# Performance work log

Measured on AMD Instinct MI355X. Metric: run time of the kernel, lower is better.

The kernel has to match this reference:

```python
import jax, jax.numpy as jnp
import numpy as np

NUM_NODES = 20000
NUM_EDGES = 65536
WIDTH = 64
EDGE_FEAT = 6
HIDDEN = 128


def setup_inputs() -> dict:
    key = jax.random.key(0)
    ks = jax.random.split(key, 6)
    x = jax.random.normal(ks[0], (NUM_NODES, WIDTH), dtype=jnp.float32)
    edge_attr = jax.random.normal(ks[1], (NUM_EDGES, EDGE_FEAT), dtype=jnp.float32)
    # weight-generating MLP params (the `nn` callable), fan-in scaled
    W1 = jax.random.normal(ks[2], (EDGE_FEAT, HIDDEN), dtype=jnp.float32) / np.sqrt(EDGE_FEAT)
    b1 = jnp.zeros((HIDDEN,), dtype=jnp.float32)
    W2 = jax.random.normal(ks[3], (HIDDEN, WIDTH * WIDTH), dtype=jnp.float32) / np.sqrt(HIDDEN)
    b2 = jnp.zeros((WIDTH * WIDTH,), dtype=jnp.float32)
    senders = jax.random.randint(ks[4], (NUM_EDGES,), 0, NUM_NODES)
    receivers = jax.random.randint(ks[5], (NUM_EDGES,), 0, NUM_NODES)
    return {"x": x, "edge_attr": edge_attr, "W1": W1, "b1": b1,
            "W2": W2, "b2": b2, "senders": senders, "receivers": receivers}


def reference(x, edge_attr, W1, b1, W2, b2, senders, receivers):
    n_segs, width = x.shape
    # nn(edge_attr): (E, width*width) edge-conditioned weights
    h = jax.nn.relu(edge_attr @ W1 + b1)
    weight = (h @ W2 + b2).reshape(-1, width, width)  # (E, w, w)
    # gather sender features, per-edge (1,w) @ (w,w) matmul -> (E, w)
    msgs = jnp.einsum('ew,ewv->ev', x[senders], weight)
    # scatter-sum messages into receiver nodes (aggr == 'sum')
    return jax.ops.segment_sum(msgs, receivers, num_segments=n_segs)
```

## Files before the change

kernel.cpp:

```cpp
#include <hip/hip_runtime.h>
#include <stdint.h>

typedef _Float16 f16;
typedef f16 f16x8 __attribute__((ext_vector_type(8)));
typedef float f32x4 __attribute__((ext_vector_type(4)));

#define NUM_NODES 20000
#define NUM_EDGES 65536
#define WIDTH 64
#define EDGE_FEAT 6
#define HIDDEN 128
#define BM 256
#define NCHUNK 129
#define XPAD 72

#define XH_HALFS (NUM_NODES * WIDTH)
#define XCONV_BLKS 625
#define W2G_HALFS (NCHUNK * 4096)
#define HT_HALFS ((size_t)NCHUNK * NUM_EDGES)
#define HBLKS (NUM_EDGES / 256)
#define OUT_FLOATS (NUM_NODES * WIDTH)
#define ZBLKS 313

__device__ __forceinline__ void gload_lds16(const f16* g, f16* l) {
  __builtin_amdgcn_global_load_lds(
      (const __attribute__((address_space(1))) unsigned int*)g,
      (__attribute__((address_space(3))) unsigned int*)l, 16, 0, 0);
}

__global__ __launch_bounds__(256) void prep_kernel(
    const float* __restrict__ x, const float* __restrict__ W2,
    const float* __restrict__ b2, const float* __restrict__ ea,
    const float* __restrict__ W1, const float* __restrict__ b1,
    f16* __restrict__ ws_h, float* __restrict__ out, int use_ht)
{
  f16* x_h = ws_h;
  f16* W2g = ws_h + XH_HALFS;
  f16* hT  = ws_h + XH_HALFS + W2G_HALFS;
  const int blk = blockIdx.x, tid = threadIdx.x;

  if (blk < NCHUNK) {
    __shared__ float row[4096];
    const int ki = blk;
    const float* srcrow;
    if (ki < HIDDEN) {
      const float4* src = (const float4*)(W2 + (size_t)ki * 4096);
      #pragma unroll
      for (int i = 0; i < 4; ++i) {
        float4 v = src[tid + 256 * i];
        *(float4*)&row[(tid + 256 * i) * 4] = v;
      }
      __syncthreads();
      srcrow = row;
    } else {
      srcrow = b2;
    }
    const int obase = tid * 16;
    f16x8 outv0, outv1;
    #pragma unroll
    for (int u = 0; u < 8; ++u) {
      int o = obase + u;
      int n = o >> 6, pg = (o >> 3) & 7, j = o & 7;
      int k = (pg ^ (n & 7)) * 8 + j;
      outv0[u] = (f16)srcrow[k * 64 + n];
    }
    #pragma unroll
    for (int u = 0; u < 8; ++u) {
      int o = obase + 8 + u;
      int n = o >> 6, pg = (o >> 3) & 7, j = o & 7;
      int k = (pg ^ (n & 7)) * 8 + j;
      outv1[u] = (f16)srcrow[k * 64 + n];
    }
    *(f16x8*)&W2g[(size_t)ki * 4096 + obase] = outv0;
    *(f16x8*)&W2g[(size_t)ki * 4096 + obase + 8] = outv1;
  } else if (blk < NCHUNK + XCONV_BLKS) {
    int idx = (blk - NCHUNK) * 2048 + tid * 8;
    if (idx + 8 <= XH_HALFS) {
      float4 a = *(const float4*)(x + idx);
      float4 b = *(const float4*)(x + idx + 4);
      f16x8 hv;
      hv[0] = (f16)a.x; hv[1] = (f16)a.y; hv[2] = (f16)a.z; hv[3] = (f16)a.w;
      hv[4] = (f16)b.x; hv[5] = (f16)b.y; hv[6] = (f16)b.z; hv[7] = (f16)b.w;
      *(f16x8*)&x_h[idx] = hv;
    }
  } else if (blk < NCHUNK + XCONV_BLKS + ZBLKS) {
    int base = (blk - NCHUNK - XCONV_BLKS) * 4096 + tid * 16;
    float4 z = {0.f, 0.f, 0.f, 0.f};
    #pragma unroll
    for (int i = 0; i < 4; ++i) {
      int idx = base + i * 4;
      if (idx + 4 <= OUT_FLOATS) *(float4*)(out + idx) = z;
    }
  } else if (use_ht) {
    __shared__ float w1s[EDGE_FEAT * HIDDEN];
    __shared__ float b1s[HIDDEN];
    for (int i = tid; i < EDGE_FEAT * HIDDEN; i += 256) w1s[i] = W1[i];
    if (tid < HIDDEN) b1s[tid] = b1[tid];
    __syncthreads();
    const int e = (blk - NCHUNK - XCONV_BLKS - ZBLKS) * 256 + tid;
    const float* p = ea + (size_t)e * EDGE_FEAT;
    float a[6];
    #pragma unroll
    for (int f = 0; f < 6; ++f) a[f] = p[f];
    #pragma unroll 4
    for (int k = 0; k < HIDDEN; ++k) {
      float s = b1s[k];
      #pragma unroll
      for (int f = 0; f < 6; ++f) s = fmaf(a[f], w1s[f * HIDDEN + k], s);
      hT[(size_t)k * NUM_EDGES + e] = (f16)fmaxf(s, 0.f);
    }
    hT[(size_t)HIDDEN * NUM_EDGES + e] = (f16)1.f;
  }
}

template<int HT>
__global__ __launch_bounds__(256, 1) void nnconv_kernel(
    const float* __restrict__ ea, const float* __restrict__ W1,
    const float* __restrict__ b1, const int* __restrict__ senders,
    const int* __restrict__ receivers, const f16* __restrict__ ws_h,
    float* __restrict__ out)
{
  const f16* x_h = ws_h;
  const f16* W2g = ws_h + XH_HALFS;
  const f16* hT  = ws_h + XH_HALFS + W2G_HALFS;
  __shared__ __align__(16) f16 xt[BM][XPAD];
  __shared__ __align__(16) f16 Bb[2][4096];

  const int tid = threadIdx.x;
  const int lane = tid & 63, wid = tid >> 6;
  const int quad = lane >> 4, l15 = lane & 15;
  const int e0 = blockIdx.x * BM;
  const int rowbase = wid * 64;

  {
    int s = senders[e0 + tid];
    const uint4* src = (const uint4*)(x_h + (size_t)s * WIDTH);
    uint4* dst = (uint4*)&xt[tid][0];
    #pragma unroll
    for (int i = 0; i < 8; ++i) dst[i] = src[i];
  }

  float ear[4][6];
  if (!HT) {
    #pragma unroll
    for (int t = 0; t < 4; ++t) {
      const float* p = ea + (size_t)(e0 + rowbase + t * 16 + l15) * EDGE_FEAT;
      #pragma unroll
      for (int f = 0; f < 6; ++f) ear[t][f] = p[f];
    }
  }

  int boff[2][4];
  #pragma unroll
  for (int kc = 0; kc < 2; ++kc)
    #pragma unroll
    for (int nt = 0; nt < 4; ++nt) {
      int n = nt * 16 + l15;
      int g = kc * 4 + quad;
      boff[kc][nt] = n * 64 + (g ^ (n & 7)) * 8;
    }

  const int hrow = e0 + rowbase + l15;
  const int stg_src = wid * 512 + (lane << 3);
  const int stg_dst = wid * 512;

  gload_lds16(W2g + stg_src, &Bb[0][stg_dst]);
  gload_lds16(W2g + 2048 + stg_src, &Bb[0][stg_dst + 2048]);
  gload_lds16(W2g + 4096 + stg_src, &Bb[1][stg_dst]);
  gload_lds16(W2g + 4096 + 2048 + stg_src, &Bb[1][stg_dst + 2048]);
  f16 hA[4], hB[4], hC[4];
  if (HT) {
    const f16* h0 = hT + hrow;
    const f16* h1 = hT + (size_t)NUM_EDGES + hrow;
    #pragma unroll
    for (int t = 0; t < 4; ++t) { hA[t] = h0[t * 16]; hB[t] = h1[t * 16]; }
  }

  __syncthreads();

  f16x8 xf[4][2];
  #pragma unroll
  for (int t = 0; t < 4; ++t)
    #pragma unroll
    for (int kc = 0; kc < 2; ++kc)
      xf[t][kc] = *(const f16x8*)&xt[rowbase + t * 16 + l15][kc * 32 + quad * 8];

  f32x4 acc[4][4];
  #pragma unroll
  for (int t = 0; t < 4; ++t)
    #pragma unroll
    for (int nt = 0; nt < 4; ++nt)
      acc[t][nt] = (f32x4){0.f, 0.f, 0.f, 0.f};

  f16x8 bfA[2][4], bfB[2][4];
  #pragma unroll
  for (int kc = 0; kc < 2; ++kc)
    #pragma unroll
    for (int nt = 0; nt < 4; ++nt)
      bfA[kc][nt] = *(const f16x8*)&Bb[0][boff[kc][nt]];

#define NN_STEP(K, CUR, NXT, DOREAD)                                          \
  {                                                                           \
    asm volatile("s_waitcnt vmcnt(%0) lgkmcnt(0)\n\ts_barrier"                \
                 :: "i"(HT ? 4 : 0) : "memory");                              \
    const int c2_ = ((K) + 2 <= 128) ? (K) + 2 : 128;                         \
    {                                                                         \
      const f16* src_ = W2g + (size_t)c2_ * 4096 + stg_src;                   \
      f16* dst_ = &Bb[(K) & 1][stg_dst];                                      \
      gload_lds16(src_, dst_);                                                \
      gload_lds16(src_ + 2048, dst_ + 2048);                                  \
    }                                                                         \
    __builtin_amdgcn_sched_barrier(0);      \
    if (HT) {                                                                 \
      const f16* hp_ = hT + (size_t)c2_ * NUM_EDGES + hrow;                   \
      hC[0] = hp_[0]; hC[1] = hp_[16]; hC[2] = hp_[32]; hC[3] = hp_[48];      \
    }                                                                         \
    if (DOREAD) {                                                             \
      f16* rb_ = &Bb[((K) + 1) & 1][0];                                       \
      _Pragma("unroll") for (int kc = 0; kc < 2; ++kc)                        \
        _Pragma("unroll") for (int nt = 0; nt < 4; ++nt)                      \
          NXT[kc][nt] = *(const f16x8*)&rb_[boff[kc][nt]];                    \
    }                                                                         \
    f16 hv_[4];                                                               \
    if (HT) {                                                                 \
      _Pragma("unroll") for (int t = 0; t < 4; ++t) hv_[t] = hA[t];           \
    } else {                                                                  \
      if ((K) < HIDDEN) {                                                     \
        float b1c_ = b1[(K)];                                                 \
        float w1c_[6];                                                        \
        _Pragma("unroll") for (int f = 0; f < 6; ++f)                         \
          w1c_[f] = W1[f * HIDDEN + (K)];                                     \
        _Pragma("unroll") for (int t = 0; t < 4; ++t) {                       \
          float s_ = b1c_;                                                    \
          _Pragma("unroll") for (int f = 0; f < 6; ++f)                       \
            s_ = fmaf(ear[t][f], w1c_[f], s_);                                \
          hv_[t] = (f16)fmaxf(s_, 0.f);                                       \
        }                                                                     \
      } else {                                                                \
        _Pragma("unroll") for (int t = 0; t < 4; ++t) hv_[t] = (f16)1.f;      \
      }                                                                       \
    }                                                                         \
    _Pragma("unroll") for (int t = 0; t < 4; ++t) {                           \
      f16x8 sa0_ = xf[t][0] * hv_[t];                                         \
      f16x8 sa1_ = xf[t][1] * hv_[t];                                         \
      _Pragma("unroll") for (int nt = 0; nt < 4; ++nt) {                      \
        acc[t][nt] = __builtin_amdgcn_mfma_f32_16x16x32_f16(                  \
            sa0_, CUR[0][nt], acc[t][nt], 0, 0, 0);                           \
        acc[t][nt] = __builtin_amdgcn_mfma_f32_16x16x32_f16(                  \
            sa1_, CUR[1][nt], acc[t][nt], 0, 0, 0);                           \
      }                                                                       \
    }                                                                         \
    if (HT) {                                                                 \
      _Pragma("unroll") for (int t = 0; t < 4; ++t) {                         \
        hA[t] = hB[t]; hB[t] = hC[t];                                         \
      }                                                                       \
    }                                                                         \
  }

  #pragma unroll 1
  for (int kb = 0; kb < 64; ++kb) {
    NN_STEP(2 * kb,     bfA, bfB, true);
    NN_STEP(2 * kb + 1, bfB, bfA, true);
  }
  NN_STEP(128, bfA, bfB, false);
#undef NN_STEP

  #pragma unroll
  for (int t = 0; t < 4; ++t) {
    int ebase = e0 + rowbase + t * 16 + quad * 4;
    int rc[4];
    #pragma unroll
    for (int r = 0; r < 4; ++r) rc[r] = receivers[ebase + r];
    #pragma unroll
    for (int nt = 0; nt < 4; ++nt) {
      int v = nt * 16 + l15;
      #pragma unroll
      for (int r = 0; r < 4; ++r)
        atomicAdd(out + (size_t)rc[r] * WIDTH + v, acc[t][nt][r]);
    }
  }
}

extern "C" void kernel_launch(void* const* d_in, const int* in_sizes, int n_in,
                              void* d_out, int out_size, void* d_ws, size_t ws_size,
                              hipStream_t stream) {
  const float* x  = (const float*)d_in[0];
  const float* ea = (const float*)d_in[1];
  const float* W1 = (const float*)d_in[2];
  const float* b1 = (const float*)d_in[3];
  const float* W2 = (const float*)d_in[4];
  const float* b2 = (const float*)d_in[5];
  const int* snd  = (const int*)d_in[6];
  const int* rcv  = (const int*)d_in[7];
  float* out = (float*)d_out;
  f16* wsh = (f16*)d_ws;

  const size_t need = ((size_t)XH_HALFS + W2G_HALFS + HT_HALFS) * sizeof(f16);
  const int use_ht = (ws_size >= need) ? 1 : 0;

  const int prep_grid = NCHUNK + XCONV_BLKS + ZBLKS + (use_ht ? HBLKS : 0);
  prep_kernel<<<prep_grid, 256, 0, stream>>>(x, W2, b2, ea, W1, b1, wsh, out, use_ht);
  if (use_ht)
    nnconv_kernel<1><<<NUM_EDGES / BM, 256, 0, stream>>>(ea, W1, b1, snd, rcv, wsh, out);
  else
    nnconv_kernel<0><<<NUM_EDGES / BM, 256, 0, stream>>>(ea, W1, b1, snd, rcv, wsh, out);
}
```

Measured before the change: 175.6 us.

## Halve edge tile and split waves over M/N halves for two blocks per CU

Shrinks the per-block edge tile from 256 to 128 and arranges the four waves as a 2x2 grid over edge rows and output columns, so each wave keeps half the accumulators and B fragments. Launch bounds now request two blocks per CU, and the grid doubles, giving more waves to hide the per-step barrier and load latency. It also reorders the hidden-value prefetch into alternating register sets, moves the LDS B-fragment reads after the h computation, and raises wave priority around the MFMA block. In exchange each W2 chunk is now staged from global memory twice as many times across the grid.

Result: no change. 176.3 us (+0.4%).

```diff
diff --git a/kernel.cpp b/kernel.cpp
--- a/kernel.cpp
+++ b/kernel.cpp
@@ -10,7 +10,7 @@
 #define WIDTH 64
 #define EDGE_FEAT 6
 #define HIDDEN 128
-#define BM 256
+#define BM 128
 #define NCHUNK 129
 #define XPAD 72
 
@@ -114,7 +114,7 @@
 }
 
 template<int HT>
-__global__ __launch_bounds__(256, 1) void nnconv_kernel(
+__global__ __launch_bounds__(256, 2) void nnconv_kernel(
     const float* __restrict__ ea, const float* __restrict__ W1,
     const float* __restrict__ b1, const int* __restrict__ senders,
     const int* __restrict__ receivers, const f16* __restrict__ ws_h,
@@ -129,51 +129,53 @@
   const int tid = threadIdx.x;
   const int lane = tid & 63, wid = tid >> 6;
   const int quad = lane >> 4, l15 = lane & 15;
+  const int mhalf = wid >> 1, nhalf = wid & 1;
   const int e0 = blockIdx.x * BM;
-  const int rowbase = wid * 64;
+  const int mbase = mhalf * 64;
 
   {
-    int s = senders[e0 + tid];
-    const uint4* src = (const uint4*)(x_h + (size_t)s * WIDTH);
-    uint4* dst = (uint4*)&xt[tid][0];
-    #pragma unroll
-    for (int i = 0; i < 8; ++i) dst[i] = src[i];
+    int r = tid >> 1, half = tid & 1;
+    int s = senders[e0 + r];
+    const uint4* src = (const uint4*)(x_h + (size_t)s * WIDTH + half * 32);
+    uint4* dst = (uint4*)&xt[r][half * 32];
+    #pragma unroll
+    for (int i = 0; i < 4; ++i) dst[i] = src[i];
   }
 
   float ear[4][6];
   if (!HT) {
     #pragma unroll
     for (int t = 0; t < 4; ++t) {
-      const float* p = ea + (size_t)(e0 + rowbase + t * 16 + l15) * EDGE_FEAT;
+      const float* p = ea + (size_t)(e0 + mbase + t * 16 + l15) * EDGE_FEAT;
       #pragma unroll
       for (int f = 0; f < 6; ++f) ear[t][f] = p[f];
     }
   }
 
-  int boff[2][4];
+  int boff[2][2];
   #pragma unroll
   for (int kc = 0; kc < 2; ++kc)
     #pragma unroll
-    for (int nt = 0; nt < 4; ++nt) {
-      int n = nt * 16 + l15;
+    for (int nt = 0; nt < 2; ++nt) {
+      int n = (nhalf * 2 + nt) * 16 + l15;
       int g = kc * 4 + quad;
       boff[kc][nt] = n * 64 + (g ^ (n & 7)) * 8;
     }
 
-  const int hrow = e0 + rowbase + l15;
+  const int hrow = e0 + mbase + l15;
   const int stg_src = wid * 512 + (lane << 3);
   const int stg_dst = wid * 512;
 
   gload_lds16(W2g + stg_src, &Bb[0][stg_dst]);
   gload_lds16(W2g + 2048 + stg_src, &Bb[0][stg_dst + 2048]);
   gload_lds16(W2g + 4096 + stg_src, &Bb[1][stg_dst]);
-  gload_lds16(W2g + 4096 + 2048 + stg_src, &Bb[1][stg_dst + 2048]);
-  f16 hA[4], hB[4], hC[4];
+  gload_lds16(W2g + 6144 + stg_src, &Bb[1][stg_dst + 2048]);
+  f16 hA[4], hB[4];
   if (HT) {
-    const f16* h0 = hT + hrow;
-    const f16* h1 = hT + (size_t)NUM_EDGES + hrow;
-    #pragma unroll
-    for (int t = 0; t < 4; ++t) { hA[t] = h0[t * 16]; hB[t] = h1[t * 16]; }
+    #pragma unroll
+    for (int t = 0; t < 4; ++t) hA[t] = hT[hrow + t * 16];
+    #pragma unroll
+    for (int t = 0; t < 4; ++t) hB[t] = hT[(size_t)NUM_EDGES + hrow + t * 16];
   }
 
   __syncthreads();
@@ -183,26 +185,27 @@
   for (int t = 0; t < 4; ++t)
     #pragma unroll
     for (int kc = 0; kc < 2; ++kc)
-      xf[t][kc] = *(const f16x8*)&xt[rowbase + t * 16 + l15][kc * 32 + quad * 8];
-
-  f32x4 acc[4][4];
+      xf[t][kc] = *(const f16x8*)&xt[mbase + t * 16 + l15][kc * 32 + quad * 8];
+
+  f32x4 acc[4][2];
   #pragma unroll
   for (int t = 0; t < 4; ++t)
     #pragma unroll
-    for (int nt = 0; nt < 4; ++nt)
+    for (int nt = 0; nt < 2; ++nt)
       acc[t][nt] = (f32x4){0.f, 0.f, 0.f, 0.f};
 
-  f16x8 bfA[2][4], bfB[2][4];
+  f16x8 bfA[2][2], bfB[2][2];
   #pragma unroll
   for (int kc = 0; kc < 2; ++kc)
     #pragma unroll
-    for (int nt = 0; nt < 4; ++nt)
+    for (int nt = 0; nt < 2; ++nt)
       bfA[kc][nt] = *(const f16x8*)&Bb[0][boff[kc][nt]];
 
-#define NN_STEP(K, CUR, NXT, DOREAD)                                          \
+#define NN_STEP(K, HS, CUR, NXT, DOREAD)                                      \
   {                                                                           \
     asm volatile("s_waitcnt vmcnt(%0) lgkmcnt(0)\n\ts_barrier"                \
                  :: "i"(HT ? 4 : 0) : "memory");                              \
+    __builtin_amdgcn_sched_barrier(0);                                        \
     const int c2_ = ((K) + 2 <= 128) ? (K) + 2 : 128;                         \
     {                                                                         \
       const f16* src_ = W2g + (size_t)c2_ * 4096 + stg_src;                   \
@@ -210,20 +213,13 @@
       gload_lds16(src_, dst_);                                                \
       gload_lds16(src_ + 2048, dst_ + 2048);                                  \
     }                                                                         \
-    __builtin_amdgcn_sched_barrier(0);      \
-    if (HT) {                                                                 \
-      const f16* hp_ = hT + (size_t)c2_ * NUM_EDGES + hrow;                   \
-      hC[0] = hp_[0]; hC[1] = hp_[16]; hC[2] = hp_[32]; hC[3] = hp_[48];      \
-    }                                                                         \
-    if (DOREAD) {                                                             \
-      f16* rb_ = &Bb[((K) + 1) & 1][0];                                       \
-      _Pragma("unroll") for (int kc = 0; kc < 2; ++kc)                        \
-        _Pragma("unroll") for (int nt = 0; nt < 4; ++nt)                      \
-          NXT[kc][nt] = *(const f16x8*)&rb_[boff[kc][nt]];                    \
-    }                                                                         \
+    __builtin_amdgcn_sched_barrier(0);         \
     f16 hv_[4];                                                               \
     if (HT) {                                                                 \
-      _Pragma("unroll") for (int t = 0; t < 4; ++t) hv_[t] = hA[t];           \
+      _Pragma("unroll") for (int t = 0; t < 4; ++t) hv_[t] = HS[t];           \
+      const f16* hp_ = hT + (size_t)c2_ * NUM_EDGES + hrow;                   \
+      HS[0] = hp_[0]; HS[1] = hp_[16]; HS[2] = hp_[32]; HS[3] = hp_[48];      \
+      __builtin_amdgcn_sched_barrier(0);             \
     } else {                                                                  \
       if ((K) < HIDDEN) {                                                     \
         float b1c_ = b1[(K)];                                                 \
@@ -240,40 +236,45 @@
         _Pragma("unroll") for (int t = 0; t < 4; ++t) hv_[t] = (f16)1.f;      \
       }                                                                       \
     }                                                                         \
+    if (DOREAD) {                                                             \
+      f16* rb_ = &Bb[((K) + 1) & 1][0];                                       \
+      _Pragma("unroll") for (int kc = 0; kc < 2; ++kc)                        \
+        _Pragma("unroll") for (int nt = 0; nt < 2; ++nt)                      \
+          NXT[kc][nt] = *(const f16x8*)&rb_[boff[kc][nt]];                    \
+    }                                                                         \
+    __builtin_amdgcn_s_setprio(1);                                            \
     _Pragma("unroll") for (int t = 0; t < 4; ++t) {                           \
       f16x8 sa0_ = xf[t][0] * hv_[t];                                         \
       f16x8 sa1_ = xf[t][1] * hv_[t];                                         \
-      _Pragma("unroll") for (int nt = 0; nt < 4; ++nt) {                      \
+      _Pragma("unroll") for (int nt = 0; nt < 2; ++nt) {                      \
         acc[t][nt] = __builtin_amdgcn_mfma_f32_16x16x32_f16(                  \
             sa0_, CUR[0][nt], acc[t][nt], 0, 0, 0);                           \
         acc[t][nt] = __builtin_amdgcn_mfma_f32_16x16x32_f16(                  \
             sa1_, CUR[1][nt], acc[t][nt], 0, 0, 0);                           \
       }                                                                       \
     }                                                                         \
-    if (HT) {                                                                 \
-      _Pragma("unroll") for (int t = 0; t < 4; ++t) {                         \
-        hA[t] = hB[t]; hB[t] = hC[t];                                         \
-      }                                                                       \
-    }                                                                         \
+    __builtin_amdgcn_s_setprio(0);                                            \
   }
 
   #pragma unroll 1
   for (int kb = 0; kb < 64; ++kb) {
-    NN_STEP(2 * kb,     bfA, bfB, true);
-    NN_STEP(2 * kb + 1, bfB, bfA, true);
-  }
-  NN_STEP(128, bfA, bfB, false);
+    NN_STEP(2 * kb,     hA, bfA, bfB, 1);
+    NN_STEP(2 * kb + 1, hB, bfB, bfA, 1);
+  }
+  NN_STEP(128, hA, bfA, bfB, 0);
 #undef NN_STEP
 
+  asm volatile("s_waitcnt vmcnt(0)" ::: "memory");
+
   #pragma unroll
   for (int t = 0; t < 4; ++t) {
-    int ebase = e0 + rowbase + t * 16 + quad * 4;
+    int ebase = e0 + mbase + t * 16 + quad * 4;
     int rc[4];
     #pragma unroll
     for (int r = 0; r < 4; ++r) rc[r] = receivers[ebase + r];
     #pragma unroll
-    for (int nt = 0; nt < 4; ++nt) {
-      int v = nt * 16 + l15;
+    for (int nt = 0; nt < 2; ++nt) {
+      int v = (nhalf * 2 + nt) * 16 + l15;
       #pragma unroll
       for (int r = 0; r < 4; ++r)
         atomicAdd(out + (size_t)rc[r] * WIDTH + v, acc[t][nt][r]);
```
